# Kernel optimization log

Measured on AMD Instinct MI355X. Metric: run time of the kernel, lower is better.

Reference implementation:

```python
import jax, jax.numpy as jnp
import numpy as np

N_NODES = 100000
N_EDGES = 1600000
D_IN = 128
D_HID = 128
D_OUT = 2
N_GRAPHS = 1024


def setup_inputs() -> dict:
    key = jax.random.key(0)
    ks = jax.random.split(key, 10)
    x = jax.random.normal(ks[0], (N_NODES, D_IN), dtype=jnp.float32)
    edge_index = jax.random.randint(ks[1], (2, N_EDGES), 0, N_NODES, dtype=jnp.int64)
    batch = jnp.sort(jax.random.randint(ks[2], (N_NODES,), 0, N_GRAPHS, dtype=jnp.int64))
    s = 1.0 / np.sqrt(D_IN)
    W1 = jax.random.uniform(ks[3], (D_IN, D_HID), jnp.float32, -s, s)
    b1 = jnp.zeros((D_HID,), jnp.float32)
    W2 = jax.random.uniform(ks[4], (D_HID, D_HID), jnp.float32, -s, s)
    b2 = jnp.zeros((D_HID,), jnp.float32)
    Wc = jax.random.uniform(ks[5], (D_HID, D_OUT), jnp.float32, -s, s)
    bc = jnp.zeros((D_OUT,), jnp.float32)
    return {"x": x, "edge_index": edge_index, "batch": batch,
            "W1": W1, "b1": b1, "W2": W2, "b2": b2, "Wc": Wc, "bc": bc}


def reference(x, edge_index, batch, W1, b1, W2, b2, Wc, bc):
    N = x.shape[0]
    # GCNConv: add self-loops, symmetric normalization D^-1/2 A D^-1/2
    loops = jnp.arange(N, dtype=edge_index.dtype)
    src = jnp.concatenate([edge_index[0], loops])
    dst = jnp.concatenate([edge_index[1], loops])
    deg = jax.ops.segment_sum(jnp.ones_like(dst, dtype=x.dtype), dst, num_segments=N)
    dinv = jnp.where(deg > 0, jax.lax.rsqrt(jnp.maximum(deg, 1e-12)), 0.0)
    norm = (dinv[src] * dinv[dst])[:, None]  # [E+N, 1]

    def gcn_conv(h, W, b):
        h = h @ W                                  # linear (no bias in PyG lin)
        msg = h[src] * norm                        # gather + scale
        agg = jax.ops.segment_sum(msg, dst, num_segments=N)  # scatter-add
        return agg + b

    h = jax.nn.relu(gcn_conv(x, W1, b1))   # dropout: inference mode (identity)
    h = jax.nn.relu(gcn_conv(h, W2, b2))
    # global_mean_pool over graph ids
    sums = jax.ops.segment_sum(h, batch, num_segments=N_GRAPHS)
    cnts = jax.ops.segment_sum(jnp.ones((N,), h.dtype), batch, num_segments=N_GRAPHS)
    pooled = sums / jnp.maximum(cnts, 1.0)[:, None]
    return pooled @ Wc + bc
```

## Files before the change

### kernel.cpp

```cpp
#include <hip/hip_runtime.h>

#define NN 100000
#define NE 1600000
#define D 128
#define NG 1024
#define SCAN_CHUNK 2048
#define NB ((NN + SCAN_CHUNK - 1) / SCAN_CHUNK)
#define GEMM_BLKS ((NN + 63) / 64)
#define HIST_BLKS ((NE + 255) / 256)
#define BOUNDS_BLKS 5

typedef _Float16 h4   __attribute__((ext_vector_type(4)));
typedef _Float16 h8   __attribute__((ext_vector_type(8)));
typedef float    f32x4 __attribute__((ext_vector_type(4)));

template<int L2>
__device__ __forceinline__ void gemm_mfma(const void* __restrict__ inv,
                                          const _Float16* __restrict__ Wt,
                                          const float* __restrict__ bias,
                                          _Float16* __restrict__ out,
                                          int blk) {
    __shared__ _Float16 wl[128][136];

    int tid = threadIdx.x;
#pragma unroll
    for (int i = 0; i < 8; ++i) {
        int s = tid + i * 256;
        int row = s >> 4, ks = s & 15;
        *(h8*)&wl[row][ks * 8] = *(const h8*)(Wt + row * D + ks * 8);
    }
    __syncthreads();

    int wv = tid >> 6, l = tid & 63;
    int li = l & 15, lg = l >> 4;
    int row0 = blk * 64;
    int colw = wv * 32;

    f32x4 acc[4][2] = {};

    const float*    inf = (const float*)inv;
    const _Float16* inh = (const _Float16*)inv;

#pragma unroll
    for (int kt = 0; kt < 4; ++kt) {
        int kb = kt * 32 + lg * 8;
        float bb[8];
        if (L2) {
#pragma unroll
            for (int e = 0; e < 8; ++e) bb[e] = bias[kb + e];
        }
        h8 a[4];
#pragma unroll
        for (int rt = 0; rt < 4; ++rt) {
            int rg = row0 + rt * 16 + li; if (rg >= NN) rg = NN - 1;
            if (L2) {
                h8 hv = *(const h8*)(inh + (size_t)rg * D + kb);
                h8 av;
#pragma unroll
                for (int e = 0; e < 8; ++e)
                    av[e] = (_Float16)fmaxf((float)hv[e] + bb[e], 0.f);
                a[rt] = av;
            } else {
                float4 f0 = *(const float4*)(inf + (size_t)rg * D + kb);
                float4 f1 = *(const float4*)(inf + (size_t)rg * D + kb + 4);
                h8 av;
                av[0] = (_Float16)f0.x; av[1] = (_Float16)f0.y;
                av[2] = (_Float16)f0.z; av[3] = (_Float16)f0.w;
                av[4] = (_Float16)f1.x; av[5] = (_Float16)f1.y;
                av[6] = (_Float16)f1.z; av[7] = (_Float16)f1.w;
                a[rt] = av;
            }
        }
#pragma unroll
        for (int ct = 0; ct < 2; ++ct) {
            h8 b = *(const h8*)&wl[colw + ct * 16 + li][kb];
#pragma unroll
            for (int rt = 0; rt < 4; ++rt)
                acc[rt][ct] = __builtin_amdgcn_mfma_f32_16x16x32_f16(
                    a[rt], b, acc[rt][ct], 0, 0, 0);
        }
    }

#pragma unroll
    for (int rt = 0; rt < 4; ++rt)
#pragma unroll
        for (int ct = 0; ct < 2; ++ct)
#pragma unroll
            for (int e = 0; e < 4; ++e) {
                int rg = row0 + rt * 16 + lg * 4 + e;
                if (rg < NN)
                    out[(size_t)rg * D + colw + ct * 16 + li] =
                        (_Float16)acc[rt][ct][e];
            }
}

__global__ __launch_bounds__(256) void k_gemm1(const float* __restrict__ x,
                                               const _Float16* __restrict__ Wt1,
                                               _Float16* __restrict__ out) {
    gemm_mfma<0>(x, Wt1, nullptr, out, blockIdx.x);
}

__global__ __launch_bounds__(256) void k_gemm2(const _Float16* __restrict__ in,
                                               const _Float16* __restrict__ Wt2,
                                               const float* __restrict__ b1,
                                               _Float16* __restrict__ out) {
    gemm_mfma<1>(in, Wt2, b1, out, blockIdx.x);
}

__global__ __launch_bounds__(256) void k_pre(const int* __restrict__ dst,
                                             int* __restrict__ deg,
                                             const float* __restrict__ W1,
                                             const float* __restrict__ W2,
                                             _Float16* __restrict__ Wt1,
                                             _Float16* __restrict__ Wt2) {
    int b = blockIdx.x;
    if (b < HIST_BLKS) {
        int e = b * 256 + threadIdx.x;
        if (e < NE) atomicAdd(&deg[dst[e]], 1);
        return;
    }
    const float*  W  = (b == HIST_BLKS) ? W1 : W2;
    _Float16*     Wt = (b == HIST_BLKS) ? Wt1 : Wt2;
    int t = threadIdx.x;
#pragma unroll
    for (int i = 0; i < 16; ++i) {
        int idx = t + i * 256;
        int k = idx >> 5, c4 = (idx & 31) * 4;
        float4 v = *(const float4*)(W + k * D + c4);
        Wt[(c4 + 0) * D + k] = (_Float16)v.x;
        Wt[(c4 + 1) * D + k] = (_Float16)v.y;
        Wt[(c4 + 2) * D + k] = (_Float16)v.z;
        Wt[(c4 + 3) * D + k] = (_Float16)v.w;
    }
}

__global__ __launch_bounds__(256) void k_scanA(const int* __restrict__ deg,
                                               float* __restrict__ dinv,
                                               int* __restrict__ row_ptr,
                                               int* __restrict__ bsum,
                                               const int* __restrict__ batch,
                                               int* __restrict__ gstart) {
    int b = blockIdx.x, tid = threadIdx.x;
    if (b >= NB) {
        int g = (b - NB) * 256 + tid;
        if (g > NG) return;
        if (g == NG) { gstart[NG] = NN; return; }
        int lo = 0, hi = NN;
        while (lo < hi) {
            int mid = (lo + hi) >> 1;
            if (batch[mid] < g) lo = mid + 1; else hi = mid;
        }
        gstart[g] = lo;
        return;
    }
    __shared__ int sh[256];
    int base = b * SCAN_CHUNK + tid * 8;
    int loc[8];
    int s = 0;
#pragma unroll
    for (int j = 0; j < 8; ++j) {
        int i = base + j;
        int d = (i < NN) ? deg[i] : 0;
        if (i < NN) dinv[i] = rsqrtf((float)(d + 1));
        loc[j] = s;
        s += d;
    }
    sh[tid] = s;
    __syncthreads();
    for (int off = 1; off < 256; off <<= 1) {
        int v = (tid >= off) ? sh[tid - off] : 0;
        __syncthreads();
        sh[tid] += v;
        __syncthreads();
    }
    int excl = (tid == 0) ? 0 : sh[tid - 1];
#pragma unroll
    for (int j = 0; j < 8; ++j) {
        int i = base + j;
        if (i < NN) row_ptr[i] = excl + loc[j];
    }
    if (tid == 255) bsum[b] = sh[255];
}

__global__ __launch_bounds__(256) void k_scanC(int* __restrict__ row_ptr,
                                               const int* __restrict__ bsum,
                                               int* __restrict__ fill) {
    __shared__ int sb[64];
    int tid = threadIdx.x;
    if (tid < NB) sb[tid] = bsum[tid];
    __syncthreads();
    int chunk = (blockIdx.x * 256) / SCAN_CHUNK;
    int pre = 0;
    for (int b = 0; b < chunk; ++b) pre += sb[b];
    int i = blockIdx.x * 256 + tid;
    if (i < NN) {
        int r = row_ptr[i] + pre;
        row_ptr[i] = r;
        fill[i] = r;
    }
    if (i == 0) row_ptr[NN] = NE;
}

__global__ __launch_bounds__(256) void k_fill(const int* __restrict__ src,
                                              const int* __restrict__ dst,
                                              const float* __restrict__ dinv,
                                              int* __restrict__ fill,
                                              int2* __restrict__ csr) {
    int e = blockIdx.x * 256 + threadIdx.x;
    if (e >= NE) return;
    int s = src[e], d = dst[e];
    float nrm = dinv[s] * dinv[d];
    int pos = atomicAdd(&fill[d], 1);
    csr[pos] = make_int2(s, __float_as_int(nrm));
}

__global__ __launch_bounds__(256) void k_gather(const _Float16* __restrict__ hh,
                                                const int* __restrict__ row_ptr,
                                                const int2* __restrict__ csr,
                                                const float* __restrict__ dinv,
                                                _Float16* __restrict__ agg) {
    int t = blockIdx.x * 256 + threadIdx.x;
    int v = t >> 5;
    if (v >= NN) return;
    int c = (t & 31) * 4;

    float di = dinv[v];
    float sl = di * di;
    h4 hv = *(const h4*)(hh + (size_t)v * D + c);
    float4 acc = make_float4((float)hv.x * sl, (float)hv.y * sl,
                             (float)hv.z * sl, (float)hv.w * sl);

    int p   = row_ptr[v];
    int end = row_ptr[v + 1];
    for (; p + 3 < end; p += 4) {
        int2 e0 = csr[p], e1 = csr[p + 1], e2 = csr[p + 2], e3 = csr[p + 3];
        float n0 = __int_as_float(e0.y);
        float n1 = __int_as_float(e1.y);
        float n2 = __int_as_float(e2.y);
        float n3 = __int_as_float(e3.y);
        h4 g0 = *(const h4*)(hh + (size_t)e0.x * D + c);
        h4 g1 = *(const h4*)(hh + (size_t)e1.x * D + c);
        h4 g2 = *(const h4*)(hh + (size_t)e2.x * D + c);
        h4 g3 = *(const h4*)(hh + (size_t)e3.x * D + c);
        acc.x += (float)g0.x * n0; acc.y += (float)g0.y * n0;
        acc.z += (float)g0.z * n0; acc.w += (float)g0.w * n0;
        acc.x += (float)g1.x * n1; acc.y += (float)g1.y * n1;
        acc.z += (float)g1.z * n1; acc.w += (float)g1.w * n1;
        acc.x += (float)g2.x * n2; acc.y += (float)g2.y * n2;
        acc.z += (float)g2.z * n2; acc.w += (float)g2.w * n2;
        acc.x += (float)g3.x * n3; acc.y += (float)g3.y * n3;
        acc.z += (float)g3.z * n3; acc.w += (float)g3.w * n3;
    }
    for (; p < end; ++p) {
        int2 e0 = csr[p];
        float n0 = __int_as_float(e0.y);
        h4 g0 = *(const h4*)(hh + (size_t)e0.x * D + c);
        acc.x += (float)g0.x * n0; acc.y += (float)g0.y * n0;
        acc.z += (float)g0.z * n0; acc.w += (float)g0.w * n0;
    }
    h4 ov = {(_Float16)acc.x, (_Float16)acc.y, (_Float16)acc.z, (_Float16)acc.w};
    *(h4*)(agg + (size_t)v * D + c) = ov;
}

__global__ __launch_bounds__(128) void k_poolcls(const _Float16* __restrict__ agg,
                                                 const float* __restrict__ b2,
                                                 const int* __restrict__ gstart,
                                                 const float* __restrict__ Wc,
                                                 const float* __restrict__ bc,
                                                 float* __restrict__ out) {
    int g = blockIdx.x;
    int c = threadIdx.x;
    int v0 = gstart[g], v1 = gstart[g + 1];
    float bb = b2[c];
    float acc = 0.f;
    int v = v0;
    for (; v + 7 < v1; v += 8) {
        float x0 = (float)agg[(size_t)(v + 0) * D + c];
        float x1 = (float)agg[(size_t)(v + 1) * D + c];
        float x2 = (float)agg[(size_t)(v + 2) * D + c];
        float x3 = (float)agg[(size_t)(v + 3) * D + c];
        float x4 = (float)agg[(size_t)(v + 4) * D + c];
        float x5 = (float)agg[(size_t)(v + 5) * D + c];
        float x6 = (float)agg[(size_t)(v + 6) * D + c];
        float x7 = (float)agg[(size_t)(v + 7) * D + c];
        acc += fmaxf(x0 + bb, 0.f) + fmaxf(x1 + bb, 0.f)
             + fmaxf(x2 + bb, 0.f) + fmaxf(x3 + bb, 0.f)
             + fmaxf(x4 + bb, 0.f) + fmaxf(x5 + bb, 0.f)
             + fmaxf(x6 + bb, 0.f) + fmaxf(x7 + bb, 0.f);
    }
    for (; v < v1; ++v)
        acc += fmaxf((float)agg[(size_t)v * D + c] + bb, 0.f);

    float inv = 1.0f / fmaxf((float)(v1 - v0), 1.0f);
    float pv = acc * inv;

    __shared__ float red[2][128];
    red[0][c] = pv * Wc[c * 2 + 0];
    red[1][c] = pv * Wc[c * 2 + 1];
    __syncthreads();
    if (c < 64) {
        float s = red[0][c] + red[0][c + 64];
        for (int off = 32; off; off >>= 1) s += __shfl_down(s, off);
        if (c == 0) out[g * 2 + 0] = s + bc[0];
    } else {
        int l = c - 64;
        float s = red[1][l] + red[1][l + 64];
        for (int off = 32; off; off >>= 1) s += __shfl_down(s, off);
        if (l == 0) out[g * 2 + 1] = s + bc[1];
    }
}

extern "C" void kernel_launch(void* const* d_in, const int* in_sizes, int n_in,
                              void* d_out, int out_size, void* d_ws, size_t ws_size,
                              hipStream_t stream) {
    const float* x     = (const float*)d_in[0];
    const int*   ei    = (const int*)d_in[1];
    const int*   batch = (const int*)d_in[2];
    const float* W1    = (const float*)d_in[3];
    const float* b1    = (const float*)d_in[4];
    const float* W2    = (const float*)d_in[5];
    const float* b2    = (const float*)d_in[6];
    const float* Wc    = (const float*)d_in[7];
    const float* bc    = (const float*)d_in[8];
    float* out = (float*)d_out;

    const int* src = ei;
    const int* dst = ei + NE;

    char* p = (char*)d_ws;
    int*       deg_i   = (int*)p;       p += 100352 * 4;
    float*     dinv    = (float*)p;     p += 100352 * 4;
    int*       row_ptr = (int*)p;       p += 100352 * 4;
    int*       fillc   = (int*)p;       p += 100352 * 4;
    int*       bsum    = (int*)p;       p += 256 * 4;
    int*       gstart  = (int*)p;       p += 1056 * 4;
    _Float16*  Wt1     = (_Float16*)p;  p += 16384 * 2;
    _Float16*  Wt2     = (_Float16*)p;  p += 16384 * 2;
    int2*      csr     = (int2*)p;      p += (size_t)NE * 8;
    _Float16*  bufA    = (_Float16*)p;  p += (size_t)NN * D * 2;
    _Float16*  bufB    = (_Float16*)p;  p += (size_t)NN * D * 2;

    hipMemsetAsync(deg_i, 0, 100352 * 4, stream);

    k_pre<<<HIST_BLKS + 2, 256, 0, stream>>>(dst, deg_i, W1, W2, Wt1, Wt2);
    k_scanA<<<NB + BOUNDS_BLKS, 256, 0, stream>>>(deg_i, dinv, row_ptr, bsum, batch, gstart);
    k_scanC<<<(NN + 255) / 256, 256, 0, stream>>>(row_ptr, bsum, fillc);
    k_fill<<<HIST_BLKS, 256, 0, stream>>>(src, dst, dinv, fillc, csr);

    k_gemm1<<<GEMM_BLKS, 256, 0, stream>>>(x, Wt1, bufA);
    k_gather<<<NN * 32 / 256, 256, 0, stream>>>(bufA, row_ptr, csr, dinv, bufB);

    k_gemm2<<<GEMM_BLKS, 256, 0, stream>>>(bufB, Wt2, b1, bufA);
    k_gather<<<NN * 32 / 256, 256, 0, stream>>>(bufA, row_ptr, csr, dinv, bufB);

    k_poolcls<<<NG, 128, 0, stream>>>(bufB, b2, gstart, Wc, bc, out);
}
```

Before: 359.5 us.

## Build CSR via two-pass bucketed scatter with shared-memory atomics

Replaces the single-pass CSR fill, which used per-node global atomics and random 8-byte writes, with two passes. The first bins edges into 256-node buckets using one global atomic counter per bucket and writes (src,dst) pairs to a staging buffer. The second places each bucket's edges using shared-memory atomics, so writes stay inside a local region and dinv lookups are partly localized. The cost is an extra kernel launch, 12.8 MB of extra traffic through the staging buffer, and heavy contention on only about 391 global bucket counters.

```diff
diff --git a/kernel.cpp b/kernel.cpp
--- a/kernel.cpp
+++ b/kernel.cpp
@@ -9,6 +9,7 @@
 #define GEMM_BLKS ((NN + 63) / 64)
 #define HIST_BLKS ((NE + 255) / 256)
 #define BOUNDS_BLKS 5
+#define NBUCK ((NN + 255) / 256)
 
 typedef _Float16 h4   __attribute__((ext_vector_type(4)));
 typedef _Float16 h8   __attribute__((ext_vector_type(8)));
@@ -184,7 +185,7 @@
 
 __global__ __launch_bounds__(256) void k_scanC(int* __restrict__ row_ptr,
                                                const int* __restrict__ bsum,
-                                               int* __restrict__ fill) {
+                                               int* __restrict__ bfill) {
     __shared__ int sb[64];
     int tid = threadIdx.x;
     if (tid < NB) sb[tid] = bsum[tid];
@@ -196,22 +197,42 @@
     if (i < NN) {
         int r = row_ptr[i] + pre;
         row_ptr[i] = r;
-        fill[i] = r;
+        if ((i & 255) == 0) bfill[i >> 8] = r;
     }
     if (i == 0) row_ptr[NN] = NE;
 }
 
-__global__ __launch_bounds__(256) void k_fill(const int* __restrict__ src,
-                                              const int* __restrict__ dst,
-                                              const float* __restrict__ dinv,
-                                              int* __restrict__ fill,
-                                              int2* __restrict__ csr) {
+__global__ __launch_bounds__(256) void k_fillA(const int* __restrict__ src,
+                                               const int* __restrict__ dst,
+                                               int* __restrict__ bfill,
+                                               int2* __restrict__ ebuf) {
     int e = blockIdx.x * 256 + threadIdx.x;
     if (e >= NE) return;
     int s = src[e], d = dst[e];
-    float nrm = dinv[s] * dinv[d];
-    int pos = atomicAdd(&fill[d], 1);
-    csr[pos] = make_int2(s, __float_as_int(nrm));
+    int pos = atomicAdd(&bfill[d >> 8], 1);
+    ebuf[pos] = make_int2(s, d);
+}
+
+__global__ __launch_bounds__(256) void k_fillB(const int2* __restrict__ ebuf,
+                                               const int* __restrict__ row_ptr,
+                                               const float* __restrict__ dinv,
+                                               int2* __restrict__ csr) {
+    __shared__ int lfill[256];
+    int b  = blockIdx.x;
+    int n0 = b << 8;
+    int t  = threadIdx.x;
+    int node = n0 + t;
+    if (node < NN) lfill[t] = row_ptr[node];
+    __syncthreads();
+    int start = row_ptr[n0];
+    int nend  = n0 + 256; if (nend > NN) nend = NN;
+    int end   = row_ptr[nend];
+    for (int p = start + t; p < end; p += 256) {
+        int2 e = ebuf[p];
+        float nrm = dinv[e.x] * dinv[e.y];
+        int pos = atomicAdd(&lfill[e.y & 255], 1);
+        csr[pos] = make_int2(e.x, __float_as_int(nrm));
+    }
 }
 
 __global__ __launch_bounds__(256) void k_gather(const _Float16* __restrict__ hh,
@@ -331,11 +352,12 @@
     int*       deg_i   = (int*)p;       p += 100352 * 4;
     float*     dinv    = (float*)p;     p += 100352 * 4;
     int*       row_ptr = (int*)p;       p += 100352 * 4;
-    int*       fillc   = (int*)p;       p += 100352 * 4;
     int*       bsum    = (int*)p;       p += 256 * 4;
     int*       gstart  = (int*)p;       p += 1056 * 4;
+    int*       bfill   = (int*)p;       p += 512 * 4;
     _Float16*  Wt1     = (_Float16*)p;  p += 16384 * 2;
     _Float16*  Wt2     = (_Float16*)p;  p += 16384 * 2;
+    int2*      ebuf    = (int2*)p;      p += (size_t)NE * 8;
     int2*      csr     = (int2*)p;      p += (size_t)NE * 8;
     _Float16*  bufA    = (_Float16*)p;  p += (size_t)NN * D * 2;
     _Float16*  bufB    = (_Float16*)p;  p += (size_t)NN * D * 2;
@@ -344,8 +366,9 @@
 
     k_pre<<<HIST_BLKS + 2, 256, 0, stream>>>(dst, deg_i, W1, W2, Wt1, Wt2);
     k_scanA<<<NB + BOUNDS_BLKS, 256, 0, stream>>>(deg_i, dinv, row_ptr, bsum, batch, gstart);
-    k_scanC<<<(NN + 255) / 256, 256, 0, stream>>>(row_ptr, bsum, fillc);
-    k_fill<<<HIST_BLKS, 256, 0, stream>>>(src, dst, dinv, fillc, csr);
+    k_scanC<<<(NN + 255) / 256, 256, 0, stream>>>(row_ptr, bsum, bfill);
+    k_fillA<<<HIST_BLKS, 256, 0, stream>>>(src, dst, bfill, ebuf);
+    k_fillB<<<NBUCK, 256, 0, stream>>>(ebuf, row_ptr, dinv, csr);
 
     k_gemm1<<<GEMM_BLKS, 256, 0, stream>>>(x, Wt1, bufA);
     k_gather<<<NN * 32 / 256, 256, 0, stream>>>(bufA, row_ptr, csr, dinv, bufB);
```

Result: slower. 855.0 us (+137.8%).
